# Performance work log

Measured on AMD Instinct MI355X. Metric: run time of the kernel, lower is better.

## Reference

```python
import jax, jax.numpy as jnp
import numpy as np

B, S, D_IN, D_OUT, H = 16, 4096, 1024, 1024, 16
HD = D_OUT // H  # 64
EPS = 1e-6


def setup_inputs() -> dict:
    key = jax.random.key(0)
    ks = jax.random.split(key, 10)
    scale = 1.0 / np.sqrt(D_OUT)
    return {
        "y_superposed": jax.random.normal(ks[0], (B, S, D_OUT), dtype=jnp.float32),
        "x_context": jax.random.normal(ks[1], (B, D_IN), dtype=jnp.float32),
        "Wq": jax.random.normal(ks[2], (D_IN, D_OUT), dtype=jnp.float32) * scale,
        "bq": jnp.zeros((D_OUT,), dtype=jnp.float32),
        "Wk": jax.random.normal(ks[3], (D_OUT, D_OUT), dtype=jnp.float32) * scale,
        "bk": jnp.zeros((D_OUT,), dtype=jnp.float32),
        "Wv": jax.random.normal(ks[4], (D_OUT, D_OUT), dtype=jnp.float32) * scale,
        "bv": jnp.zeros((D_OUT,), dtype=jnp.float32),
        "Wo": jax.random.normal(ks[5], (D_OUT, D_OUT), dtype=jnp.float32) * scale,
        "bo": jnp.zeros((D_OUT,), dtype=jnp.float32),
    }


def _feature_map(x):
    # feature_map_id == 1: elu(x) + 1 (strictly positive kernel feature map)
    return jax.nn.elu(x) + 1.0


def reference(y_superposed, x_context, Wq, bq, Wk, bk, Wv, bv, Wo, bo):
    b = x_context.shape[0]
    # Q from context: [b, d_out] -> [b, H, 1, hd]
    q = (x_context @ Wq + bq).reshape(b, 1, H, HD).transpose(0, 2, 1, 3)
    # K, V from superposed states: [b, S, d_out] -> [b, H, S, hd]
    k = (y_superposed @ Wk + bk).reshape(b, -1, H, HD).transpose(0, 2, 1, 3)
    v = (y_superposed @ Wv + bv).reshape(b, -1, H, HD).transpose(0, 2, 1, 3)
    # Kernel (linear) attention: O(S) path, elu+1 feature map
    phi_q = _feature_map(q)          # [b, H, 1, hd]
    phi_k = _feature_map(k)          # [b, H, S, hd]
    kv = jnp.einsum('bhsd,bhsv->bhdv', phi_k, v)        # [b, H, hd, hd]
    numerator = jnp.einsum('bhqd,bhdv->bhqv', phi_q, kv)  # [b, H, 1, hd]
    k_sum = jnp.sum(phi_k, axis=2, keepdims=True)        # [b, H, 1, hd]
    denominator = jnp.sum(phi_q * k_sum, axis=-1, keepdims=True)  # [b, H, 1, 1]
    ctx = numerator / (denominator + EPS)                # [b, H, 1, hd]
    # Collapse heads back: [b, H, 1, hd] -> [b, d_out]
    ctx = ctx.transpose(0, 2, 1, 3).reshape(b, D_OUT)
    return ctx @ Wo + bo
```

## Files before the change

kernel.cpp:

```cpp
#include <hip/hip_runtime.h>

#define D   1024
#define S   4096
#define NB  16
#define NH  16
#define NSC 16

using bf16x8 = __attribute__((ext_vector_type(8))) short;
using f32x4  = __attribute__((ext_vector_type(4))) float;

__device__ __forceinline__ short f2bf(float f) {
    unsigned int u = __float_as_uint(f);
    u += 0x7fffu + ((u >> 16) & 1u);
    return (short)(u >> 16);
}
__device__ __forceinline__ float bf2f(unsigned short u) {
    return __uint_as_float(((unsigned int)u) << 16);
}
__device__ __forceinline__ float elu1(float x) {
    return x > 0.f ? x + 1.f : __expf(x);
}

__global__ __launch_bounds__(256) void ybf_kernel(const float* __restrict__ y,
        unsigned short* __restrict__ ybf)
{
    const size_t stride = (size_t)gridDim.x * 256 * 4;
    size_t idx = ((size_t)blockIdx.x * 256 + threadIdx.x) * 4;
    const size_t total = (size_t)NB * S * D;
    for (; idx < total; idx += stride) {
        const float4 v = *reinterpret_cast<const float4*>(y + idx);
        short4 p;
        p.x = f2bf(v.x); p.y = f2bf(v.y); p.z = f2bf(v.z); p.w = f2bf(v.w);
        *reinterpret_cast<short4*>(ybf + idx) = p;
    }
}

__global__ __launch_bounds__(256) void phiq_kernel(const float* __restrict__ x,
        const float* __restrict__ Wq, const float* __restrict__ bq,
        float* __restrict__ phiq)
{
    const int b = blockIdx.y;
    const int o = blockIdx.x * 256 + threadIdx.x;
    __shared__ float xl[D];
    for (int i = threadIdx.x; i < D; i += 256) xl[i] = x[b * D + i];
    __syncthreads();
    float acc = bq[o];
    for (int j = 0; j < D; ++j) acc = fmaf(xl[j], Wq[(size_t)j * D + o], acc);
    phiq[b * D + o] = elu1(acc);
}

__global__ __launch_bounds__(256) void wkt_kernel(const float* __restrict__ Wk,
        unsigned short* __restrict__ WkT)
{
    __shared__ float tile[32][33];
    const int tx = threadIdx.x & 31, ty = threadIdx.x >> 5;
    const int j0 = blockIdx.y * 32, o0 = blockIdx.x * 32;
#pragma unroll
    for (int r = 0; r < 4; ++r)
        tile[ty + r * 8][tx] = Wk[(size_t)(j0 + ty + r * 8) * D + o0 + tx];
    __syncthreads();
#pragma unroll
    for (int r = 0; r < 4; ++r) {
        const int o = o0 + ty + r * 8;
        WkT[(size_t)o * D + j0 + tx] = (unsigned short)f2bf(tile[tx][ty + r * 8]);
    }
}

__global__ __launch_bounds__(256, 2) void kgemm_kernel(
        const unsigned short* __restrict__ ybf, const unsigned short* __restrict__ WkT,
        const float* __restrict__ phiq, const float* __restrict__ bk,
        float* __restrict__ wbuf)
{
    const int bid = blockIdx.x;
    const int wg  = (bid & 7) * 256 + (bid >> 3);
    const int mt  = wg >> 2;
    const int nt  = wg & 3;
    const int b   = mt >> 5;
    const int s0  = (mt & 31) << 7;
    const int n0  = nt << 8;
    const int t   = threadIdx.x;
    const int wv  = t >> 6;
    const int l   = t & 63;
    const int wr  = wv >> 1, wc = wv & 1;
    const int l15 = l & 15, l16 = l >> 4;

    __shared__ short Al[128 * 64];
    __shared__ short Bl[256 * 64];

    f32x4 acc[4][8] = {};

    const unsigned short* yb = ybf + (size_t)(b * S + s0) * D;

    for (int kt = 0; kt < D / 64; ++kt) {
        const int k0 = kt * 64;
#pragma unroll
        for (int i = 0; i < 4; ++i) {
            const int slot0 = i * 256 + wv * 64;
            const int slot  = slot0 + l;
            const int row   = slot >> 3;
            const int ke    = ((slot & 7) ^ (row & 7)) << 3;
            __builtin_amdgcn_global_load_lds(
                (const __attribute__((address_space(1))) unsigned int*)(yb + (size_t)row * D + k0 + ke),
                (__attribute__((address_space(3))) unsigned int*)(&Al[slot0 * 8]),
                16, 0, 0);
        }
#pragma unroll
        for (int i = 0; i < 8; ++i) {
            const int slot0 = i * 256 + wv * 64;
            const int slot  = slot0 + l;
            const int nrow  = slot >> 3;
            const int ke    = ((slot & 7) ^ (nrow & 7)) << 3;
            __builtin_amdgcn_global_load_lds(
                (const __attribute__((address_space(1))) unsigned int*)(WkT + (size_t)(n0 + nrow) * D + k0 + ke),
                (__attribute__((address_space(3))) unsigned int*)(&Bl[slot0 * 8]),
                16, 0, 0);
        }
        __syncthreads();
#pragma unroll
        for (int kk = 0; kk < 2; ++kk) {
            bf16x8 af[4], bfr[8];
            const int ks = (kk << 2) + l16;
#pragma unroll
            for (int m = 0; m < 4; ++m) {
                const int row = wr * 64 + m * 16 + l15;
                af[m] = *reinterpret_cast<const bf16x8*>(&Al[row * 64 + ((ks ^ (row & 7)) << 3)]);
            }
#pragma unroll
            for (int n = 0; n < 8; ++n) {
                const int row = wc * 128 + n * 16 + l15;
                bfr[n] = *reinterpret_cast<const bf16x8*>(&Bl[row * 64 + ((ks ^ (row & 7)) << 3)]);
            }
#pragma unroll
            for (int m = 0; m < 4; ++m)
#pragma unroll
                for (int n = 0; n < 8; ++n)
                    acc[m][n] = __builtin_amdgcn_mfma_f32_16x16x32_bf16(af[m], bfr[n], acc[m][n], 0, 0, 0);
        }
        __syncthreads();
    }

    const int h0 = (n0 >> 6) + wc * 2;
    float pq[8], bkv[8];
#pragma unroll
    for (int n = 0; n < 8; ++n) {
        const int col = n0 + wc * 128 + n * 16 + l15;
        pq[n]  = phiq[b * D + col];
        bkv[n] = bk[col];
    }
#pragma unroll
    for (int m = 0; m < 4; ++m) {
#pragma unroll
        for (int j = 0; j < 4; ++j) {
            float rs0 = 0.f, rs1 = 0.f;
#pragma unroll
            for (int n = 0; n < 4; ++n) {
                rs0 += elu1(acc[m][n][j] + bkv[n]) * pq[n];
                rs1 += elu1(acc[m][n + 4][j] + bkv[n + 4]) * pq[n + 4];
            }
            rs0 += __shfl_xor(rs0, 1); rs1 += __shfl_xor(rs1, 1);
            rs0 += __shfl_xor(rs0, 2); rs1 += __shfl_xor(rs1, 2);
            rs0 += __shfl_xor(rs0, 4); rs1 += __shfl_xor(rs1, 4);
            rs0 += __shfl_xor(rs0, 8); rs1 += __shfl_xor(rs1, 8);
            if (l15 == 0) {
                const int row = s0 + wr * 64 + m * 16 + l16 * 4 + j;
                wbuf[(size_t)(b * NH + h0) * S + row]     = rs0;
                wbuf[(size_t)(b * NH + h0 + 1) * S + row] = rs1;
            }
        }
    }
}

__global__ __launch_bounds__(256) void tpart_kernel(
        const unsigned short* __restrict__ ybf, const float* __restrict__ wbuf,
        float* __restrict__ tpart)
{
    const int sc = blockIdx.x;
    const int b  = blockIdx.y;
    const int t  = threadIdx.x;
    const int s0 = sc * 256;
    __shared__ float wl[16 * 256];
#pragma unroll
    for (int r = 0; r < 16; ++r) {
        const int lin = r * 256 + t;
        wl[lin] = wbuf[(size_t)(b * NH + (lin >> 8)) * S + s0 + (lin & 255)];
    }
    __syncthreads();
    float acc[16][4] = {};
    const unsigned short* yb = ybf + (size_t)(b * S + s0) * D + t * 4;
    for (int si = 0; si < 256; ++si) {
        const short4 v4 = *reinterpret_cast<const short4*>(yb + (size_t)si * D);
        const float vx = bf2f((unsigned short)v4.x);
        const float vy = bf2f((unsigned short)v4.y);
        const float vz = bf2f((unsigned short)v4.z);
        const float vw = bf2f((unsigned short)v4.w);
#pragma unroll
        for (int hh = 0; hh < 16; ++hh) {
            const float wv = wl[hh * 256 + si];
            acc[hh][0] = fmaf(wv, vx, acc[hh][0]);
            acc[hh][1] = fmaf(wv, vy, acc[hh][1]);
            acc[hh][2] = fmaf(wv, vz, acc[hh][2]);
            acc[hh][3] = fmaf(wv, vw, acc[hh][3]);
        }
    }
    float* tp = tpart + ((size_t)(sc * NB + b) * NH) * D + t * 4;
#pragma unroll
    for (int hh = 0; hh < 16; ++hh) {
        float4 o;
        o.x = acc[hh][0]; o.y = acc[hh][1]; o.z = acc[hh][2]; o.w = acc[hh][3];
        *reinterpret_cast<float4*>(tp + hh * D) = o;
    }
}

__global__ __launch_bounds__(256) void tred_kernel(const float* __restrict__ tpart,
        float* __restrict__ tbuf)
{
    const int idx = blockIdx.x * 256 + threadIdx.x;
    float s = 0.f;
#pragma unroll
    for (int sc = 0; sc < NSC; ++sc) s += tpart[(size_t)sc * (NB * NH * D) + idx];
    tbuf[idx] = s;
}

__global__ __launch_bounds__(256) void ctx_kernel(
        const float* __restrict__ wbuf, const float* __restrict__ tbuf,
        const float* __restrict__ Wv, const float* __restrict__ bv,
        float* __restrict__ ctx)
{
    const int b = blockIdx.x >> 4, h = blockIdx.x & 15;
    const int t = threadIdx.x;
    const int v = t & 63, jq = t >> 6;
    __shared__ float rnum[256];
    __shared__ float rden[4];
    const float* wr_ = wbuf + (size_t)(b * NH + h) * S;
    float dp = 0.f;
    for (int i = t; i < S; i += 256) dp += wr_[i];
#pragma unroll
    for (int off = 1; off < 64; off <<= 1) dp += __shfl_xor(dp, off);
    if ((t & 63) == 0) rden[t >> 6] = dp;
    const float* tr = tbuf + (size_t)(b * NH + h) * D;
    float np = 0.f;
    for (int j = jq * 256; j < jq * 256 + 256; ++j)
        np = fmaf(tr[j], Wv[(size_t)j * D + h * 64 + v], np);
    rnum[t] = np;
    __syncthreads();
    if (t < 64) {
        const float denom = rden[0] + rden[1] + rden[2] + rden[3];
        float num = rnum[v] + rnum[64 + v] + rnum[128 + v] + rnum[192 + v];
        num += denom * bv[h * 64 + v];
        ctx[(size_t)b * D + h * 64 + v] = num / (denom + 1e-6f);
    }
}

__global__ __launch_bounds__(256) void out_kernel(
        const float* __restrict__ ctx, const float* __restrict__ Wo,
        const float* __restrict__ bo, float* __restrict__ out)
{
    const int b = blockIdx.y;
    const int o = blockIdx.x * 256 + threadIdx.x;
    __shared__ float cl[D];
    for (int i = threadIdx.x; i < D; i += 256) cl[i] = ctx[(size_t)b * D + i];
    __syncthreads();
    float acc = bo[o];
    for (int j = 0; j < D; ++j) acc = fmaf(cl[j], Wo[(size_t)j * D + o], acc);
    out[(size_t)b * D + o] = acc;
}

extern "C" void kernel_launch(void* const* d_in, const int* in_sizes, int n_in,
                              void* d_out, int out_size, void* d_ws, size_t ws_size,
                              hipStream_t stream) {
    const float* y  = (const float*)d_in[0];
    const float* x  = (const float*)d_in[1];
    const float* Wq = (const float*)d_in[2];
    const float* bq = (const float*)d_in[3];
    const float* Wk = (const float*)d_in[4];
    const float* bk = (const float*)d_in[5];
    const float* Wv = (const float*)d_in[6];
    const float* bv = (const float*)d_in[7];
    const float* Wo = (const float*)d_in[8];
    const float* bo = (const float*)d_in[9];
    float* out = (float*)d_out;

    char* ws = (char*)d_ws;
    size_t off = 0;
    unsigned short* ybf  = (unsigned short*)(ws + off); off += (size_t)NB * S * D * 2;
    unsigned short* WkT  = (unsigned short*)(ws + off); off += (size_t)D * D * 2;
    float*          phiq = (float*)(ws + off);          off += (size_t)NB * D * 4;
    float*          wbuf = (float*)(ws + off);          off += (size_t)NB * NH * S * 4;
    float*          tpart= (float*)(ws + off);          off += (size_t)NSC * NB * NH * D * 4;
    float*          tbuf = (float*)(ws + off);          off += (size_t)NB * NH * D * 4;
    float*          ctx  = (float*)(ws + off);          off += (size_t)NB * D * 4;

    ybf_kernel <<<2048, 256, 0, stream>>>(y, ybf);
    phiq_kernel<<<dim3(4, NB), 256, 0, stream>>>(x, Wq, bq, phiq);
    wkt_kernel <<<dim3(32, 32), 256, 0, stream>>>(Wk, WkT);
    kgemm_kernel<<<2048, 256, 0, stream>>>(ybf, WkT, phiq, bk, wbuf);
    tpart_kernel<<<dim3(NSC, NB), 256, 0, stream>>>(ybf, wbuf, tpart);
    tred_kernel <<<1024, 256, 0, stream>>>(tpart, tbuf);
    ctx_kernel  <<<256, 256, 0, stream>>>(wbuf, tbuf, Wv, bv, ctx);
    out_kernel  <<<dim3(4, NB), 256, 0, stream>>>(ctx, Wo, bo, out);
}
```

Baseline: 382.5 us.

## Fuse weighted-sum of y into K-GEMM epilogue and split-K the small GEMVs

Folds the tpart and tred stages into the kgemm kernel's epilogue. Each block stages its per-row head weights in LDS, then accumulates weighted sums of its own y tile for its 4 heads, writing per-chunk partials and denominator partials. ctx_kernel now reduces these 32 partials itself. phiq and out GEMVs are split over 4 wave-groups along the reduction dimension with 16 blocks in x, to expose more parallelism. This removes a full second pass over the bf16 y buffer plus the wbuf round trip and two launches. The cost is extra epilogue work and register pressure in the GEMM, and redundant y reads, since 4 column-tile blocks each re-read the same rows.

```diff
diff --git a/kernel.cpp b/kernel.cpp
--- a/kernel.cpp
+++ b/kernel.cpp
@@ -4,7 +4,7 @@
 #define S   4096
 #define NB  16
 #define NH  16
-#define NSC 16
+#define NSC 32
 
 using bf16x8 = __attribute__((ext_vector_type(8))) short;
 using f32x4  = __attribute__((ext_vector_type(4))) float;
@@ -39,14 +39,24 @@
         const float* __restrict__ Wq, const float* __restrict__ bq,
         float* __restrict__ phiq)
 {
-    const int b = blockIdx.y;
-    const int o = blockIdx.x * 256 + threadIdx.x;
+    const int b  = blockIdx.y;
+    const int o0 = blockIdx.x * 64;
+    const int t  = threadIdx.x;
+    const int ol = t & 63, jq = t >> 6;
     __shared__ float xl[D];
-    for (int i = threadIdx.x; i < D; i += 256) xl[i] = x[b * D + i];
-    __syncthreads();
-    float acc = bq[o];
-    for (int j = 0; j < D; ++j) acc = fmaf(xl[j], Wq[(size_t)j * D + o], acc);
-    phiq[b * D + o] = elu1(acc);
+    __shared__ float rnum[256];
+    for (int i = t; i < D; i += 256) xl[i] = x[b * D + i];
+    __syncthreads();
+    float acc = 0.f;
+    const int o = o0 + ol;
+    for (int j = jq * 256; j < jq * 256 + 256; ++j)
+        acc = fmaf(xl[j], Wq[(size_t)j * D + o], acc);
+    rnum[t] = acc;
+    __syncthreads();
+    if (t < 64) {
+        float s = rnum[t] + rnum[64 + t] + rnum[128 + t] + rnum[192 + t];
+        phiq[b * D + o0 + t] = elu1(s + bq[o0 + t]);
+    }
 }
 
 __global__ __launch_bounds__(256) void wkt_kernel(const float* __restrict__ Wk,
@@ -69,7 +79,7 @@
 __global__ __launch_bounds__(256, 2) void kgemm_kernel(
         const unsigned short* __restrict__ ybf, const unsigned short* __restrict__ WkT,
         const float* __restrict__ phiq, const float* __restrict__ bk,
-        float* __restrict__ wbuf)
+        float* __restrict__ tpart, float* __restrict__ dpart)
 {
     const int bid = blockIdx.x;
     const int wg  = (bid & 7) * 256 + (bid >> 3);
@@ -139,115 +149,101 @@
         __syncthreads();
     }
 
-    const int h0 = (n0 >> 6) + wc * 2;
-    float pq[8], bkv[8];
-#pragma unroll
-    for (int n = 0; n < 8; ++n) {
-        const int col = n0 + wc * 128 + n * 16 + l15;
-        pq[n]  = phiq[b * D + col];
-        bkv[n] = bk[col];
-    }
-#pragma unroll
-    for (int m = 0; m < 4; ++m) {
-#pragma unroll
-        for (int j = 0; j < 4; ++j) {
-            float rs0 = 0.f, rs1 = 0.f;
-#pragma unroll
-            for (int n = 0; n < 4; ++n) {
-                rs0 += elu1(acc[m][n][j] + bkv[n]) * pq[n];
-                rs1 += elu1(acc[m][n + 4][j] + bkv[n + 4]) * pq[n + 4];
+    float* wsm = (float*)Al;
+    {
+        float pq[8], bkv[8];
+#pragma unroll
+        for (int n = 0; n < 8; ++n) {
+            const int col = n0 + wc * 128 + n * 16 + l15;
+            pq[n]  = phiq[b * D + col];
+            bkv[n] = bk[col];
+        }
+#pragma unroll
+        for (int m = 0; m < 4; ++m) {
+#pragma unroll
+            for (int j = 0; j < 4; ++j) {
+                float rs0 = 0.f, rs1 = 0.f;
+#pragma unroll
+                for (int n = 0; n < 4; ++n) {
+                    rs0 += elu1(acc[m][n][j] + bkv[n]) * pq[n];
+                    rs1 += elu1(acc[m][n + 4][j] + bkv[n + 4]) * pq[n + 4];
+                }
+                rs0 += __shfl_xor(rs0, 1); rs1 += __shfl_xor(rs1, 1);
+                rs0 += __shfl_xor(rs0, 2); rs1 += __shfl_xor(rs1, 2);
+                rs0 += __shfl_xor(rs0, 4); rs1 += __shfl_xor(rs1, 4);
+                rs0 += __shfl_xor(rs0, 8); rs1 += __shfl_xor(rs1, 8);
+                if (l15 == 0) {
+                    const int r = wr * 64 + m * 16 + l16 * 4 + j;
+                    wsm[r * 4 + wc * 2]     = rs0;
+                    wsm[r * 4 + wc * 2 + 1] = rs1;
+                }
             }
-            rs0 += __shfl_xor(rs0, 1); rs1 += __shfl_xor(rs1, 1);
-            rs0 += __shfl_xor(rs0, 2); rs1 += __shfl_xor(rs1, 2);
-            rs0 += __shfl_xor(rs0, 4); rs1 += __shfl_xor(rs1, 4);
-            rs0 += __shfl_xor(rs0, 8); rs1 += __shfl_xor(rs1, 8);
-            if (l15 == 0) {
-                const int row = s0 + wr * 64 + m * 16 + l16 * 4 + j;
-                wbuf[(size_t)(b * NH + h0) * S + row]     = rs0;
-                wbuf[(size_t)(b * NH + h0 + 1) * S + row] = rs1;
+        }
+    }
+    __syncthreads();
+
+    {
+        const int hw = wv;
+        const int hg = nt * 4 + hw;
+        const int j0 = l * 16;
+        float tl[16] = {};
+        float dsum = 0.f;
+        const unsigned short* ys = yb + j0;
+        for (int r = 0; r < 128; ++r) {
+            const float wv_ = wsm[r * 4 + hw];
+            dsum += wv_;
+            const bf16x8 v0 = *reinterpret_cast<const bf16x8*>(ys + (size_t)r * D);
+            const bf16x8 v1 = *reinterpret_cast<const bf16x8*>(ys + (size_t)r * D + 8);
+#pragma unroll
+            for (int i = 0; i < 8; ++i) {
+                tl[i]     = fmaf(wv_, bf2f((unsigned short)v0[i]), tl[i]);
+                tl[8 + i] = fmaf(wv_, bf2f((unsigned short)v1[i]), tl[8 + i]);
             }
         }
-    }
-}
-
-__global__ __launch_bounds__(256) void tpart_kernel(
-        const unsigned short* __restrict__ ybf, const float* __restrict__ wbuf,
-        float* __restrict__ tpart)
-{
-    const int sc = blockIdx.x;
-    const int b  = blockIdx.y;
-    const int t  = threadIdx.x;
-    const int s0 = sc * 256;
-    __shared__ float wl[16 * 256];
-#pragma unroll
-    for (int r = 0; r < 16; ++r) {
-        const int lin = r * 256 + t;
-        wl[lin] = wbuf[(size_t)(b * NH + (lin >> 8)) * S + s0 + (lin & 255)];
-    }
-    __syncthreads();
-    float acc[16][4] = {};
-    const unsigned short* yb = ybf + (size_t)(b * S + s0) * D + t * 4;
-    for (int si = 0; si < 256; ++si) {
-        const short4 v4 = *reinterpret_cast<const short4*>(yb + (size_t)si * D);
-        const float vx = bf2f((unsigned short)v4.x);
-        const float vy = bf2f((unsigned short)v4.y);
-        const float vz = bf2f((unsigned short)v4.z);
-        const float vw = bf2f((unsigned short)v4.w);
-#pragma unroll
-        for (int hh = 0; hh < 16; ++hh) {
-            const float wv = wl[hh * 256 + si];
-            acc[hh][0] = fmaf(wv, vx, acc[hh][0]);
-            acc[hh][1] = fmaf(wv, vy, acc[hh][1]);
-            acc[hh][2] = fmaf(wv, vz, acc[hh][2]);
-            acc[hh][3] = fmaf(wv, vw, acc[hh][3]);
-        }
-    }
-    float* tp = tpart + ((size_t)(sc * NB + b) * NH) * D + t * 4;
-#pragma unroll
-    for (int hh = 0; hh < 16; ++hh) {
-        float4 o;
-        o.x = acc[hh][0]; o.y = acc[hh][1]; o.z = acc[hh][2]; o.w = acc[hh][3];
-        *reinterpret_cast<float4*>(tp + hh * D) = o;
-    }
-}
-
-__global__ __launch_bounds__(256) void tred_kernel(const float* __restrict__ tpart,
-        float* __restrict__ tbuf)
-{
-    const int idx = blockIdx.x * 256 + threadIdx.x;
-    float s = 0.f;
-#pragma unroll
-    for (int sc = 0; sc < NSC; ++sc) s += tpart[(size_t)sc * (NB * NH * D) + idx];
-    tbuf[idx] = s;
+        const int sc = mt & 31;
+        float* tp = tpart + ((size_t)((sc * NB + b) * NH + hg)) * D + j0;
+#pragma unroll
+        for (int q = 0; q < 4; ++q) {
+            float4 o;
+            o.x = tl[q * 4]; o.y = tl[q * 4 + 1]; o.z = tl[q * 4 + 2]; o.w = tl[q * 4 + 3];
+            *reinterpret_cast<float4*>(tp + q * 4) = o;
+        }
+        if (l == 0) dpart[(size_t)(sc * NB + b) * NH + hg] = dsum;
+    }
 }
 
 __global__ __launch_bounds__(256) void ctx_kernel(
-        const float* __restrict__ wbuf, const float* __restrict__ tbuf,
+        const float* __restrict__ tpart, const float* __restrict__ dpart,
         const float* __restrict__ Wv, const float* __restrict__ bv,
         float* __restrict__ ctx)
 {
     const int b = blockIdx.x >> 4, h = blockIdx.x & 15;
     const int t = threadIdx.x;
+    __shared__ float t_l[D];
+    __shared__ float dl[NSC];
+    __shared__ float rnum[256];
+    if (t < NSC) dl[t] = dpart[(size_t)(t * NB + b) * NH + h];
+    float4 a = {0.f, 0.f, 0.f, 0.f};
+    for (int sc = 0; sc < NSC; ++sc) {
+        const float4 v = *reinterpret_cast<const float4*>(
+            tpart + ((size_t)((sc * NB + b) * NH + h)) * D + t * 4);
+        a.x += v.x; a.y += v.y; a.z += v.z; a.w += v.w;
+    }
+    *reinterpret_cast<float4*>(&t_l[t * 4]) = a;
+    __syncthreads();
+    float denom = 0.f;
+#pragma unroll
+    for (int i = 0; i < NSC; ++i) denom += dl[i];
     const int v = t & 63, jq = t >> 6;
-    __shared__ float rnum[256];
-    __shared__ float rden[4];
-    const float* wr_ = wbuf + (size_t)(b * NH + h) * S;
-    float dp = 0.f;
-    for (int i = t; i < S; i += 256) dp += wr_[i];
-#pragma unroll
-    for (int off = 1; off < 64; off <<= 1) dp += __shfl_xor(dp, off);
-    if ((t & 63) == 0) rden[t >> 6] = dp;
-    const float* tr = tbuf + (size_t)(b * NH + h) * D;
     float np = 0.f;
     for (int j = jq * 256; j < jq * 256 + 256; ++j)
-        np = fmaf(tr[j], Wv[(size_t)j * D + h * 64 + v], np);
+        np = fmaf(t_l[j], Wv[(size_t)j * D + h * 64 + v], np);
     rnum[t] = np;
     __syncthreads();
     if (t < 64) {
-        const float denom = rden[0] + rden[1] + rden[2] + rden[3];
-        float num = rnum[v] + rnum[64 + v] + rnum[128 + v] + rnum[192 + v];
-        num += denom * bv[h * 64 + v];
-        ctx[(size_t)b * D + h * 64 + v] = num / (denom + 1e-6f);
+        float num = rnum[t] + rnum[64 + t] + rnum[128 + t] + rnum[192 + t];
+        num += denom * bv[h * 64 + t];
+        ctx[(size_t)b * D + h * 64 + t] = num / (denom + 1e-6f);
     }
 }
 
@@ -255,14 +251,24 @@
         const float* __restrict__ ctx, const float* __restrict__ Wo,
         const float* __restrict__ bo, float* __restrict__ out)
 {
-    const int b = blockIdx.y;
-    const int o = blockIdx.x * 256 + threadIdx.x;
+    const int b  = blockIdx.y;
+    const int o0 = blockIdx.x * 64;
+    const int t  = threadIdx.x;
+    const int ol = t & 63, jq = t >> 6;
     __shared__ float cl[D];
-    for (int i = threadIdx.x; i < D; i += 256) cl[i] = ctx[(size_t)b * D + i];
-    __syncthreads();
-    float acc = bo[o];
-    for (int j = 0; j < D; ++j) acc = fmaf(cl[j], Wo[(size_t)j * D + o], acc);
-    out[(size_t)b * D + o] = acc;
+    __shared__ float rnum[256];
+    for (int i = t; i < D; i += 256) cl[i] = ctx[(size_t)b * D + i];
+    __syncthreads();
+    float acc = 0.f;
+    const int o = o0 + ol;
+    for (int j = jq * 256; j < jq * 256 + 256; ++j)
+        acc = fmaf(cl[j], Wo[(size_t)j * D + o], acc);
+    rnum[t] = acc;
+    __syncthreads();
+    if (t < 64) {
+        float s = rnum[t] + rnum[64 + t] + rnum[128 + t] + rnum[192 + t];
+        out[(size_t)b * D + o0 + t] = s + bo[o0 + t];
+    }
 }
 
 extern "C" void kernel_launch(void* const* d_in, const int* in_sizes, int n_in,
@@ -285,17 +291,14 @@
     unsigned short* ybf  = (unsigned short*)(ws + off); off += (size_t)NB * S * D * 2;
     unsigned short* WkT  = (unsigned short*)(ws + off); off += (size_t)D * D * 2;
     float*          phiq = (float*)(ws + off);          off += (size_t)NB * D * 4;
-    float*          wbuf = (float*)(ws + off);          off += (size_t)NB * NH * S * 4;
     float*          tpart= (float*)(ws + off);          off += (size_t)NSC * NB * NH * D * 4;
-    float*          tbuf = (float*)(ws + off);          off += (size_t)NB * NH * D * 4;
+    float*          dpart= (float*)(ws + off);          off += (size_t)NSC * NB * NH * 4;
     float*          ctx  = (float*)(ws + off);          off += (size_t)NB * D * 4;
 
     ybf_kernel <<<2048, 256, 0, stream>>>(y, ybf);
-    phiq_kernel<<<dim3(4, NB), 256, 0, stream>>>(x, Wq, bq, phiq);
+    phiq_kernel<<<dim3(16, NB), 256, 0, stream>>>(x, Wq, bq, phiq);
     wkt_kernel <<<dim3(32, 32), 256, 0, stream>>>(Wk, WkT);
-    kgemm_kernel<<<2048, 256, 0, stream>>>(ybf, WkT, phiq, bk, wbuf);
-    tpart_kernel<<<dim3(NSC, NB), 256, 0, stream>>>(ybf, wbuf, tpart);
-    tred_kernel <<<1024, 256, 0, stream>>>(tpart, tbuf);
-    ctx_kernel  <<<256, 256, 0, stream>>>(wbuf, tbuf, Wv, bv, ctx);
-    out_kernel  <<<dim3(4, NB), 256, 0, stream>>>(ctx, Wo, bo, out);
-}
+    kgemm_kernel<<<2048, 256, 0, stream>>>(ybf, WkT, phiq, bk, tpart, dpart);
+    ctx_kernel  <<<256, 256, 0, stream>>>(tpart, dpart, Wv, bv, ctx);
+    out_kernel  <<<dim3(16, NB), 256, 0, stream>>>(ctx, Wo, bo, out);
+}
```

Result: slower. 581.4 us (+52.0%).

## Merge prep kernels into one launch, fold partial reduction into ctx, split GEMV K

Applied to the files above, without the earlier changes.

Combines the bf16 conversion of y, the phi(q) GEMV and the Wk transpose into a single prep_kernel, dispatched by block-index range. Removes the separate tpart reduction kernel by summing the partials inside ctx_kernel into shared memory. Restructures the small GEMVs (phiq and out) to split the K dimension across four waves with a shared-memory reduction, giving more blocks per GEMV. This cuts launch count and raises parallelism in the tiny GEMVs, at the cost of more block-uniform branching in the fused kernel.

```diff
diff --git a/kernel.cpp b/kernel.cpp
--- a/kernel.cpp
+++ b/kernel.cpp
@@ -21,48 +21,58 @@
     return x > 0.f ? x + 1.f : __expf(x);
 }
 
-__global__ __launch_bounds__(256) void ybf_kernel(const float* __restrict__ y,
-        unsigned short* __restrict__ ybf)
-{
-    const size_t stride = (size_t)gridDim.x * 256 * 4;
-    size_t idx = ((size_t)blockIdx.x * 256 + threadIdx.x) * 4;
-    const size_t total = (size_t)NB * S * D;
-    for (; idx < total; idx += stride) {
-        const float4 v = *reinterpret_cast<const float4*>(y + idx);
-        short4 p;
-        p.x = f2bf(v.x); p.y = f2bf(v.y); p.z = f2bf(v.z); p.w = f2bf(v.w);
-        *reinterpret_cast<short4*>(ybf + idx) = p;
-    }
-}
-
-__global__ __launch_bounds__(256) void phiq_kernel(const float* __restrict__ x,
-        const float* __restrict__ Wq, const float* __restrict__ bq,
-        float* __restrict__ phiq)
-{
-    const int b = blockIdx.y;
-    const int o = blockIdx.x * 256 + threadIdx.x;
-    __shared__ float xl[D];
-    for (int i = threadIdx.x; i < D; i += 256) xl[i] = x[b * D + i];
-    __syncthreads();
-    float acc = bq[o];
-    for (int j = 0; j < D; ++j) acc = fmaf(xl[j], Wq[(size_t)j * D + o], acc);
-    phiq[b * D + o] = elu1(acc);
-}
-
-__global__ __launch_bounds__(256) void wkt_kernel(const float* __restrict__ Wk,
-        unsigned short* __restrict__ WkT)
-{
+__global__ __launch_bounds__(256) void prep_kernel(
+        const float* __restrict__ y, unsigned short* __restrict__ ybf,
+        const float* __restrict__ x, const float* __restrict__ Wq,
+        const float* __restrict__ bq, float* __restrict__ phiq,
+        const float* __restrict__ Wk, unsigned short* __restrict__ WkT)
+{
+    const int bid = blockIdx.x;
+    const int t   = threadIdx.x;
+    __shared__ float smemf[D];
+    __shared__ float rnum[256];
     __shared__ float tile[32][33];
-    const int tx = threadIdx.x & 31, ty = threadIdx.x >> 5;
-    const int j0 = blockIdx.y * 32, o0 = blockIdx.x * 32;
-#pragma unroll
-    for (int r = 0; r < 4; ++r)
-        tile[ty + r * 8][tx] = Wk[(size_t)(j0 + ty + r * 8) * D + o0 + tx];
-    __syncthreads();
-#pragma unroll
-    for (int r = 0; r < 4; ++r) {
-        const int o = o0 + ty + r * 8;
-        WkT[(size_t)o * D + j0 + tx] = (unsigned short)f2bf(tile[tx][ty + r * 8]);
+
+    if (bid < 2048) {
+        const size_t stride = (size_t)2048 * 256 * 4;
+        size_t idx = ((size_t)bid * 256 + t) * 4;
+        const size_t total = (size_t)NB * S * D;
+        for (; idx < total; idx += stride) {
+            const float4 v = *reinterpret_cast<const float4*>(y + idx);
+            short4 p;
+            p.x = f2bf(v.x); p.y = f2bf(v.y); p.z = f2bf(v.z); p.w = f2bf(v.w);
+            *reinterpret_cast<short4*>(ybf + idx) = p;
+        }
+    } else if (bid < 2304) {
+        const int b2 = bid - 2048;
+        const int b  = b2 >> 4;
+        const int o0 = (b2 & 15) * 64;
+        const int ol = t & 63, jq = t >> 6;
+        for (int i = t; i < D; i += 256) smemf[i] = x[b * D + i];
+        __syncthreads();
+        float acc = 0.f;
+        const int o = o0 + ol;
+        for (int j = jq * 256; j < jq * 256 + 256; ++j)
+            acc = fmaf(smemf[j], Wq[(size_t)j * D + o], acc);
+        rnum[t] = acc;
+        __syncthreads();
+        if (t < 64) {
+            float s = rnum[t] + rnum[64 + t] + rnum[128 + t] + rnum[192 + t];
+            phiq[b * D + o0 + t] = elu1(s + bq[o0 + t]);
+        }
+    } else {
+        const int b3 = bid - 2304;
+        const int j0 = (b3 >> 5) * 32, o0 = (b3 & 31) * 32;
+        const int tx = t & 31, ty = t >> 5;
+#pragma unroll
+        for (int r = 0; r < 4; ++r)
+            tile[ty + r * 8][tx] = Wk[(size_t)(j0 + ty + r * 8) * D + o0 + tx];
+        __syncthreads();
+#pragma unroll
+        for (int r = 0; r < 4; ++r) {
+            const int o = o0 + ty + r * 8;
+            WkT[(size_t)o * D + j0 + tx] = (unsigned short)f2bf(tile[tx][ty + r * 8]);
+        }
     }
 }
 
@@ -211,24 +221,14 @@
     }
 }
 
-__global__ __launch_bounds__(256) void tred_kernel(const float* __restrict__ tpart,
-        float* __restrict__ tbuf)
-{
-    const int idx = blockIdx.x * 256 + threadIdx.x;
-    float s = 0.f;
-#pragma unroll
-    for (int sc = 0; sc < NSC; ++sc) s += tpart[(size_t)sc * (NB * NH * D) + idx];
-    tbuf[idx] = s;
-}
-
 __global__ __launch_bounds__(256) void ctx_kernel(
-        const float* __restrict__ wbuf, const float* __restrict__ tbuf,
+        const float* __restrict__ wbuf, const float* __restrict__ tpart,
         const float* __restrict__ Wv, const float* __restrict__ bv,
         float* __restrict__ ctx)
 {
     const int b = blockIdx.x >> 4, h = blockIdx.x & 15;
     const int t = threadIdx.x;
-    const int v = t & 63, jq = t >> 6;
+    __shared__ float t_l[D];
     __shared__ float rnum[256];
     __shared__ float rden[4];
     const float* wr_ = wbuf + (size_t)(b * NH + h) * S;
@@ -237,17 +237,25 @@
 #pragma unroll
     for (int off = 1; off < 64; off <<= 1) dp += __shfl_xor(dp, off);
     if ((t & 63) == 0) rden[t >> 6] = dp;
-    const float* tr = tbuf + (size_t)(b * NH + h) * D;
+    float4 a = {0.f, 0.f, 0.f, 0.f};
+    for (int sc = 0; sc < NSC; ++sc) {
+        const float4 v = *reinterpret_cast<const float4*>(
+            tpart + ((size_t)((sc * NB + b) * NH + h)) * D + t * 4);
+        a.x += v.x; a.y += v.y; a.z += v.z; a.w += v.w;
+    }
+    *reinterpret_cast<float4*>(&t_l[t * 4]) = a;
+    __syncthreads();
+    const float denom = rden[0] + rden[1] + rden[2] + rden[3];
+    const int v = t & 63, jq = t >> 6;
     float np = 0.f;
     for (int j = jq * 256; j < jq * 256 + 256; ++j)
-        np = fmaf(tr[j], Wv[(size_t)j * D + h * 64 + v], np);
+        np = fmaf(t_l[j], Wv[(size_t)j * D + h * 64 + v], np);
     rnum[t] = np;
     __syncthreads();
     if (t < 64) {
-        const float denom = rden[0] + rden[1] + rden[2] + rden[3];
-        float num = rnum[v] + rnum[64 + v] + rnum[128 + v] + rnum[192 + v];
-        num += denom * bv[h * 64 + v];
-        ctx[(size_t)b * D + h * 64 + v] = num / (denom + 1e-6f);
+        float num = rnum[t] + rnum[64 + t] + rnum[128 + t] + rnum[192 + t];
+        num += denom * bv[h * 64 + t];
+        ctx[(size_t)b * D + h * 64 + t] = num / (denom + 1e-6f);
     }
 }
 
@@ -255,14 +263,24 @@
         const float* __restrict__ ctx, const float* __restrict__ Wo,
         const float* __restrict__ bo, float* __restrict__ out)
 {
-    const int b = blockIdx.y;
-    const int o = blockIdx.x * 256 + threadIdx.x;
+    const int b  = blockIdx.y;
+    const int o0 = blockIdx.x * 64;
+    const int t  = threadIdx.x;
+    const int ol = t & 63, jq = t >> 6;
     __shared__ float cl[D];
-    for (int i = threadIdx.x; i < D; i += 256) cl[i] = ctx[(size_t)b * D + i];
-    __syncthreads();
-    float acc = bo[o];
-    for (int j = 0; j < D; ++j) acc = fmaf(cl[j], Wo[(size_t)j * D + o], acc);
-    out[(size_t)b * D + o] = acc;
+    __shared__ float rnum[256];
+    for (int i = t; i < D; i += 256) cl[i] = ctx[(size_t)b * D + i];
+    __syncthreads();
+    float acc = 0.f;
+    const int o = o0 + ol;
+    for (int j = jq * 256; j < jq * 256 + 256; ++j)
+        acc = fmaf(cl[j], Wo[(size_t)j * D + o], acc);
+    rnum[t] = acc;
+    __syncthreads();
+    if (t < 64) {
+        float s = rnum[t] + rnum[64 + t] + rnum[128 + t] + rnum[192 + t];
+        out[(size_t)b * D + o0 + t] = s + bo[o0 + t];
+    }
 }
 
 extern "C" void kernel_launch(void* const* d_in, const int* in_sizes, int n_in,
@@ -287,15 +305,11 @@
     float*          phiq = (float*)(ws + off);          off += (size_t)NB * D * 4;
     float*          wbuf = (float*)(ws + off);          off += (size_t)NB * NH * S * 4;
     float*          tpart= (float*)(ws + off);          off += (size_t)NSC * NB * NH * D * 4;
-    float*          tbuf = (float*)(ws + off);          off += (size_t)NB * NH * D * 4;
     float*          ctx  = (float*)(ws + off);          off += (size_t)NB * D * 4;
 
-    ybf_kernel <<<2048, 256, 0, stream>>>(y, ybf);
-    phiq_kernel<<<dim3(4, NB), 256, 0, stream>>>(x, Wq, bq, phiq);
-    wkt_kernel <<<dim3(32, 32), 256, 0, stream>>>(Wk, WkT);
+    prep_kernel <<<3328, 256, 0, stream>>>(y, ybf, x, Wq, bq, phiq, Wk, WkT);
     kgemm_kernel<<<2048, 256, 0, stream>>>(ybf, WkT, phiq, bk, wbuf);
     tpart_kernel<<<dim3(NSC, NB), 256, 0, stream>>>(ybf, wbuf, tpart);
-    tred_kernel <<<1024, 256, 0, stream>>>(tpart, tbuf);
-    ctx_kernel  <<<256, 256, 0, stream>>>(wbuf, tbuf, Wv, bv, ctx);
-    out_kernel  <<<dim3(4, NB), 256, 0, stream>>>(ctx, Wo, bo, out);
-}
+    ctx_kernel  <<<256, 256, 0, stream>>>(wbuf, tpart, Wv, bv, ctx);
+    out_kernel  <<<dim3(16, NB), 256, 0, stream>>>(ctx, Wo, bo, out);
+}
```

Result: slower. 565.4 us (+47.8%).
